# Optimization experiments

Hardware: AMD Instinct MI355X
Metric: run time of the kernel (lower is better)

## Reference

```python
import jax, jax.numpy as jnp
import numpy as np

N = 100000       # num nodes
E = 1600000      # num edges (avg degree 16)
IN, HID, OUT, C = 128, 64, 64, 16


def setup_inputs() -> dict:
    key = jax.random.key(0)
    ks = jax.random.split(key, 10)
    x = jax.random.normal(ks[0], (N, IN), jnp.float32)
    edge_index = jax.random.randint(ks[1], (2, E), 0, N, dtype=jnp.int32)
    dict_node = jax.random.randint(ks[2], (N,), 0, N, dtype=jnp.int32)
    # learned parameters (Glorot-ish scaling)
    W1 = jax.random.normal(ks[3], (IN, HID), jnp.float32) / np.sqrt(IN)
    b1 = jnp.zeros((HID,), jnp.float32)
    W2 = jax.random.normal(ks[4], (HID, OUT), jnp.float32) / np.sqrt(HID)
    b2 = jnp.zeros((OUT,), jnp.float32)
    Wfc = jax.random.normal(ks[5], (OUT, C), jnp.float32) / np.sqrt(OUT)
    bfc = jnp.zeros((C,), jnp.float32)
    return {"x": x, "edge_index": edge_index, "dict_node": dict_node,
            "W1": W1, "b1": b1, "W2": W2, "b2": b2, "Wfc": Wfc, "bfc": bfc}


def _gcn_conv(h_in, W, b, src, dst, n):
    """GCNConv: D^-1/2 (A+I) D^-1/2 (X W) + b, self-loops handled analytically."""
    h = h_in @ W                                   # [N, F]
    deg = jax.ops.segment_sum(jnp.ones((src.shape[0],), h.dtype), dst,
                              num_segments=n) + 1.0  # +1 self-loop
    dinv = jax.lax.rsqrt(deg)                      # [N]
    norm = dinv[src] * dinv[dst]                   # [E]
    agg = jax.ops.segment_sum(h[src] * norm[:, None], dst, num_segments=n)
    agg = agg + h * (dinv * dinv)[:, None]         # self-loop contribution
    return agg + b


def reference(x, edge_index, dict_node, W1, b1, W2, b2, Wfc, bfc):
    n = x.shape[0]
    src, dst = edge_index[0], edge_index[1]
    h = jax.nn.relu(_gcn_conv(x, W1, b1, src, dst, n))
    # dropout p=0.5 is identity at inference
    h = jax.nn.relu(_gcn_conv(h, W2, b2, src, dst, n))
    # global_mean_pool over dict_node with size = num_nodes
    cnt = jax.ops.segment_sum(jnp.ones((n,), h.dtype), dict_node, num_segments=n)
    summ = jax.ops.segment_sum(h, dict_node, num_segments=n)
    pooled = summ / jnp.maximum(cnt, 1.0)[:, None]
    logits = pooled @ Wfc + bfc
    return jax.nn.log_softmax(logits, axis=1)
```

## Files before the change

### kernel.cpp

```cpp
#include <hip/hip_runtime.h>

#define THREADS 256
#define KC 32
#define B1 256

typedef __attribute__((ext_vector_type(8))) short bf16x8;
typedef __attribute__((ext_vector_type(4))) float f32x4;
typedef __attribute__((ext_vector_type(2))) unsigned int u32x2;

__device__ inline ushort f2bf(float v) {
    union { float f; unsigned u; } a; a.f = v;
    unsigned r = a.u + 0x7fff + ((a.u >> 16) & 1);
    return (ushort)(r >> 16);
}
__device__ inline unsigned pack2(float a, float b) {
    return (unsigned)f2bf(a) | ((unsigned)f2bf(b) << 16);
}
__device__ inline float bflo(unsigned v) {
    union { unsigned u; float f; } a; a.u = v << 16; return a.f;
}
__device__ inline float bfhi(unsigned v) {
    union { unsigned u; float f; } a; a.u = v & 0xffff0000u; return a.f;
}


__global__ void k_p1(const int* __restrict__ dst, int* __restrict__ pc,
                     int E, int NB, int chunk) {
    __shared__ int hist[512];
    int tid = threadIdx.x, blk = blockIdx.x;
    for (int i = tid; i < NB; i += THREADS) hist[i] = 0;
    __syncthreads();
    int e0 = blk * chunk;
    int e1 = e0 + chunk; if (e1 > E) e1 = E;
    for (int e = e0 + tid; e < e1; e += THREADS)
        atomicAdd(&hist[dst[e] >> 8], 1);
    __syncthreads();
    for (int i = tid; i < NB; i += THREADS) pc[i * B1 + blk] = hist[i];
}

__global__ void k_s1(int* __restrict__ pc, int* __restrict__ bsums, int total) {
    __shared__ int s[1024];
    int t = threadIdx.x;
    int idx = blockIdx.x * 1024 + t;
    int v = (idx < total) ? pc[idx] : 0;
    s[t] = v;
    __syncthreads();
    for (int o = 1; o < 1024; o <<= 1) {
        int x = (t >= (unsigned)o) ? s[t - o] : 0;
        __syncthreads();
        s[t] += x;
        __syncthreads();
    }
    if (idx < total) pc[idx] = s[t] - v;
    if (t == 1023) bsums[blockIdx.x] = s[1023];
}

__global__ void k_s2(int* __restrict__ bsums, int nb) {
    __shared__ int s[128];
    int t = threadIdx.x;
    int v = (t < nb) ? bsums[t] : 0;
    s[t] = v;
    __syncthreads();
    for (int o = 1; o < 128; o <<= 1) {
        int x = (t >= (unsigned)o) ? s[t - o] : 0;
        __syncthreads();
        s[t] += x;
        __syncthreads();
    }
    if (t < nb) bsums[t] = s[t] - v;
}

__global__ void k_p2(const int* __restrict__ src, const int* __restrict__ dst,
                     const int* __restrict__ pc, const int* __restrict__ bsx,
                     unsigned long long* __restrict__ part, int E, int NB, int chunk) {
    __shared__ int cur[512];
    int tid = threadIdx.x, blk = blockIdx.x;
    for (int i = tid; i < NB; i += THREADS) {
        int idx = i * B1 + blk;
        cur[i] = pc[idx] + bsx[idx >> 10];
    }
    __syncthreads();
    int e0 = blk * chunk;
    int e1 = e0 + chunk; if (e1 > E) e1 = E;
    for (int e = e0 + tid; e < e1; e += THREADS) {
        int d = dst[e], sv = src[e];
        int pos = atomicAdd(&cur[d >> 8], 1);
        part[pos] = ((unsigned long long)(unsigned)d << 32) | (unsigned)sv;
    }
}

__global__ void k_p3(const unsigned long long* __restrict__ part,
                     const int* __restrict__ pc, const int* __restrict__ bsx,
                     int* __restrict__ off, float* __restrict__ dinv,
                     int* __restrict__ csr, int E, int NB, int n) {
    __shared__ int hist[256];
    __shared__ int so[256];
    int b = blockIdx.x, t = threadIdx.x;
    int i0 = b * B1, i1 = (b + 1) * B1;
    int base = pc[i0] + bsx[i0 >> 10];
    int end  = (b + 1 < NB) ? (pc[i1] + bsx[i1 >> 10]) : E;
    hist[t] = 0;
    __syncthreads();
    for (int e = base + t; e < end; e += THREADS)
        atomicAdd(&hist[(int)(part[e] >> 32) & 255], 1);
    __syncthreads();
    int h = hist[t];
    so[t] = h;
    __syncthreads();
    for (int o = 1; o < 256; o <<= 1) {
        int x = (t >= (unsigned)o) ? so[t - o] : 0;
        __syncthreads();
        so[t] += x;
        __syncthreads();
    }
    int ex = so[t] - h;
    int node = (b << 8) + t;
    if (node < n) {
        off[node]  = base + ex;
        dinv[node] = rsqrtf((float)h + 1.0f);
        if (node == n - 1) off[n] = E;
    }
    __syncthreads();
    so[t] = base + ex;
    __syncthreads();
    for (int e = base + t; e < end; e += THREADS) {
        unsigned long long p = part[e];
        int pos = atomicAdd(&so[(int)(p >> 32) & 255], 1);
        csr[pos] = (int)(p & 0xffffffffu);
    }
}

__global__ __launch_bounds__(THREADS) void
k_g1(const float* __restrict__ X, const float* __restrict__ W,
     const float* __restrict__ dinv, ushort* __restrict__ C, int n, int fin,
     const int* __restrict__ dict, float* __restrict__ cnt, int nGemm, int nCnt) {
    int tid = threadIdx.x;
    if ((int)blockIdx.x >= nGemm) {
        int stride = nCnt * THREADS;
        for (int i = ((int)blockIdx.x - nGemm) * THREADS + tid; i < n; i += stride)
            atomicAdd(&cnt[dict[i]], 1.0f);
        return;
    }
    __shared__ float Xs[KC][68];
    __shared__ float Ws[KC][64];
    int r0  = blockIdx.x * 64;
    int tx4 = (tid & 15) * 4;
    int ty4 = (tid >> 4) * 4;
    int sxr = tid >> 2, sxk = (tid & 3) * 4;
    int swk = tid >> 4, swc = (tid & 15) * 4;
    int xrow = r0 + sxr; if (xrow >= n) xrow = n - 1;
    const float* xptr = X + (size_t)xrow * fin;
    float4 acc0 = {0,0,0,0}, acc1 = {0,0,0,0}, acc2 = {0,0,0,0}, acc3 = {0,0,0,0};
    for (int kc = 0; kc < fin; kc += KC) {
        float4 xa = *(const float4*)(xptr + kc + sxk);
        float4 xb = *(const float4*)(xptr + kc + 16 + sxk);
        float4 wa = *(const float4*)(W + (size_t)(kc + swk) * 64 + swc);
        float4 wb = *(const float4*)(W + (size_t)(kc + swk + 16) * 64 + swc);
        __syncthreads();
        Xs[sxk + 0][sxr] = xa.x; Xs[sxk + 1][sxr] = xa.y;
        Xs[sxk + 2][sxr] = xa.z; Xs[sxk + 3][sxr] = xa.w;
        Xs[16 + sxk + 0][sxr] = xb.x; Xs[16 + sxk + 1][sxr] = xb.y;
        Xs[16 + sxk + 2][sxr] = xb.z; Xs[16 + sxk + 3][sxr] = xb.w;
        *(float4*)&Ws[swk][swc]      = wa;
        *(float4*)&Ws[swk + 16][swc] = wb;
        __syncthreads();
        #pragma unroll 8
        for (int k = 0; k < KC; ++k) {
            float4 a = *(const float4*)&Xs[k][ty4];
            float4 b = *(const float4*)&Ws[k][tx4];
            acc0.x = fmaf(a.x, b.x, acc0.x); acc0.y = fmaf(a.x, b.y, acc0.y);
            acc0.z = fmaf(a.x, b.z, acc0.z); acc0.w = fmaf(a.x, b.w, acc0.w);
            acc1.x = fmaf(a.y, b.x, acc1.x); acc1.y = fmaf(a.y, b.y, acc1.y);
            acc1.z = fmaf(a.y, b.z, acc1.z); acc1.w = fmaf(a.y, b.w, acc1.w);
            acc2.x = fmaf(a.z, b.x, acc2.x); acc2.y = fmaf(a.z, b.y, acc2.y);
            acc2.z = fmaf(a.z, b.z, acc2.z); acc2.w = fmaf(a.z, b.w, acc2.w);
            acc3.x = fmaf(a.w, b.x, acc3.x); acc3.y = fmaf(a.w, b.y, acc3.y);
            acc3.z = fmaf(a.w, b.z, acc3.z); acc3.w = fmaf(a.w, b.w, acc3.w);
        }
    }
    int row = r0 + ty4;
    #pragma unroll
    for (int r = 0; r < 4; ++r) {
        if (row + r >= n) break;
        float dn = dinv[row + r];
        float4 a = r == 0 ? acc0 : r == 1 ? acc1 : r == 2 ? acc2 : acc3;
        ushort4 o;
        o.x = f2bf(a.x * dn); o.y = f2bf(a.y * dn);
        o.z = f2bf(a.z * dn); o.w = f2bf(a.w * dn);
        *(ushort4*)(C + (size_t)(row + r) * 64 + tx4) = o;
    }
}

__global__ __launch_bounds__(THREADS) void
k_gemm_bf16(const ushort* __restrict__ X, const float* __restrict__ W,
            const float* __restrict__ dinv, ushort* __restrict__ C, int n, int fin) {
    __shared__ float Xs[KC][68];
    __shared__ float Ws[KC][64];
    int tid = threadIdx.x;
    int r0  = blockIdx.x * 64;
    int tx4 = (tid & 15) * 4;
    int ty4 = (tid >> 4) * 4;
    int sxr = tid >> 2, sk8 = (tid & 3) * 8;
    int swk = tid >> 4, swc = (tid & 15) * 4;
    int xrow = r0 + sxr; if (xrow >= n) xrow = n - 1;
    const ushort* xptr = X + (size_t)xrow * fin;
    float4 acc0 = {0,0,0,0}, acc1 = {0,0,0,0}, acc2 = {0,0,0,0}, acc3 = {0,0,0,0};
    for (int kc = 0; kc < fin; kc += KC) {
        uint4 xv = *(const uint4*)(xptr + kc + sk8);
        float4 wa = *(const float4*)(W + (size_t)(kc + swk) * 64 + swc);
        float4 wb = *(const float4*)(W + (size_t)(kc + swk + 16) * 64 + swc);
        __syncthreads();
        Xs[sk8 + 0][sxr] = bflo(xv.x); Xs[sk8 + 1][sxr] = bfhi(xv.x);
        Xs[sk8 + 2][sxr] = bflo(xv.y); Xs[sk8 + 3][sxr] = bfhi(xv.y);
        Xs[sk8 + 4][sxr] = bflo(xv.z); Xs[sk8 + 5][sxr] = bfhi(xv.z);
        Xs[sk8 + 6][sxr] = bflo(xv.w); Xs[sk8 + 7][sxr] = bfhi(xv.w);
        *(float4*)&Ws[swk][swc]      = wa;
        *(float4*)&Ws[swk + 16][swc] = wb;
        __syncthreads();
        #pragma unroll 8
        for (int k = 0; k < KC; ++k) {
            float4 a = *(const float4*)&Xs[k][ty4];
            float4 b = *(const float4*)&Ws[k][tx4];
            acc0.x = fmaf(a.x, b.x, acc0.x); acc0.y = fmaf(a.x, b.y, acc0.y);
            acc0.z = fmaf(a.x, b.z, acc0.z); acc0.w = fmaf(a.x, b.w, acc0.w);
            acc1.x = fmaf(a.y, b.x, acc1.x); acc1.y = fmaf(a.y, b.y, acc1.y);
            acc1.z = fmaf(a.y, b.z, acc1.z); acc1.w = fmaf(a.y, b.w, acc1.w);
            acc2.x = fmaf(a.z, b.x, acc2.x); acc2.y = fmaf(a.z, b.y, acc2.y);
            acc2.z = fmaf(a.z, b.z, acc2.z); acc2.w = fmaf(a.z, b.w, acc2.w);
            acc3.x = fmaf(a.w, b.x, acc3.x); acc3.y = fmaf(a.w, b.y, acc3.y);
            acc3.z = fmaf(a.w, b.z, acc3.z); acc3.w = fmaf(a.w, b.w, acc3.w);
        }
    }
    int row = r0 + ty4;
    #pragma unroll
    for (int r = 0; r < 4; ++r) {
        if (row + r >= n) break;
        float dn = dinv[row + r];
        float4 a = r == 0 ? acc0 : r == 1 ? acc1 : r == 2 ? acc2 : acc3;
        ushort4 o;
        o.x = f2bf(a.x * dn); o.y = f2bf(a.y * dn);
        o.z = f2bf(a.z * dn); o.w = f2bf(a.w * dn);
        *(ushort4*)(C + (size_t)(row + r) * 64 + tx4) = o;
    }
}

__device__ inline void tr_mfma4(unsigned la, const bf16x8& a,
                                f32x4& o0, f32x4& o1, f32x4& o2, f32x4& o3) {
    u32x2 r0, r1, r2, r3, r4, r5, r6, r7;
    asm volatile(
        "s_waitcnt lgkmcnt(0)\n\t"
        "ds_read_b64_tr_b16 %0, %8 offset:0\n\t"
        "ds_read_b64_tr_b16 %1, %8 offset:512\n\t"
        "ds_read_b64_tr_b16 %2, %8 offset:1024\n\t"
        "ds_read_b64_tr_b16 %3, %8 offset:1536\n\t"
        "ds_read_b64_tr_b16 %4, %8 offset:2048\n\t"
        "ds_read_b64_tr_b16 %5, %8 offset:2560\n\t"
        "ds_read_b64_tr_b16 %6, %8 offset:3072\n\t"
        "ds_read_b64_tr_b16 %7, %8 offset:3584\n\t"
        "s_waitcnt lgkmcnt(0)"
        : "=&v"(r0), "=&v"(r1), "=&v"(r2), "=&v"(r3),
          "=&v"(r4), "=&v"(r5), "=&v"(r6), "=&v"(r7)
        : "v"(la) : "memory");
    __builtin_amdgcn_sched_barrier(0);
    union { u32x2 d[2]; bf16x8 v; } b0, b1, b2, b3;
    b0.d[0] = r0; b0.d[1] = r1; b1.d[0] = r2; b1.d[1] = r3;
    b2.d[0] = r4; b2.d[1] = r5; b3.d[0] = r6; b3.d[1] = r7;
    o0 = __builtin_amdgcn_mfma_f32_16x16x32_bf16(a, b0.v, o0, 0, 0, 0);
    o1 = __builtin_amdgcn_mfma_f32_16x16x32_bf16(a, b1.v, o1, 0, 0, 0);
    o2 = __builtin_amdgcn_mfma_f32_16x16x32_bf16(a, b2.v, o2, 0, 0, 0);
    o3 = __builtin_amdgcn_mfma_f32_16x16x32_bf16(a, b3.v, o3, 0, 0, 0);
}

template<int LAYER>
__global__ __launch_bounds__(THREADS) void
k_agg(const ushort* __restrict__ H, const int* __restrict__ csr,
      const int* __restrict__ off, const float* __restrict__ dinv,
      const float* __restrict__ bias, ushort* __restrict__ outB,
      const float* __restrict__ Wfc, const int* __restrict__ dict,
      float* __restrict__ pool16, int n) {
    __shared__ ushort cbuf[4][2048];
    __shared__ float wt[16 * 65];
    int tid = threadIdx.x;
    if (LAYER == 2) {
        for (int i = tid; i < 64 * 16; i += THREADS) {
            int cc = i >> 4, r = i & 15;
            wt[r * 65 + cc] = Wfc[i];
        }
        __syncthreads();
    }
    int wslot = tid >> 6, lane = tid & 63;
    int gw = blockIdx.x * 4 + wslot;
    int n0 = gw << 4;
    if (n0 >= n) return;
    int G = lane >> 4, c16 = lane & 15;
    int g8 = lane >> 3, q = lane & 7;
    ushort* wbuf = &cbuf[wslot][0];
    unsigned lbase = (unsigned)(size_t)wbuf;
    int vm = n - n0; if (vm > 16) vm = 16;
    int sA = 0, eA = 0;
    if (c16 < vm) { sA = off[n0 + c16]; eA = off[n0 + c16 + 1]; }
    int base0   = __shfl(sA, 0);
    int baseEnd = __shfl(eA, vm - 1);
    unsigned rng = (unsigned)(eA - sA);
    int sb0 = (q >> 1) * 512 + (g8 >> 2) * 256 + (g8 & 3) * 16 + (q & 1) * 8;
    unsigned la = lbase + (unsigned)lane * 8;
    f32x4 acc0 = {0, 0, 0, 0}, acc1 = acc0, acc2 = acc0, acc3 = acc0;

    uint4 cur[4], nxt[4];
    #pragma unroll
    for (int it = 0; it < 4; ++it) {
        uint4 v = {0, 0, 0, 0};
        int k = it * 8 + g8;
        if (base0 + k < baseEnd) {
            int e = csr[base0 + k];
            v = *(const uint4*)(H + ((size_t)e << 6) + q * 8);
        }
        cur[it] = v;
    }
    for (int base = base0; base < baseEnd; base += 32) {
        #pragma unroll
        for (int it = 0; it < 4; ++it) {
            uint4 v = {0, 0, 0, 0};
            int k = base + 32 + it * 8 + g8;
            if (k < baseEnd) {
                int e = csr[k];
                v = *(const uint4*)(H + ((size_t)e << 6) + q * 8);
            }
            nxt[it] = v;
        }
        #pragma unroll
        for (int it = 0; it < 4; ++it)
            *(uint4*)(wbuf + sb0 + it * 64) = cur[it];
        int kb = base - sA;
        bf16x8 a;
        #pragma unroll
        for (int e2 = 0; e2 < 8; ++e2)
            a[e2] = ((unsigned)(G * 8 + e2 + kb) < rng) ? (short)0x3F80 : (short)0;
        tr_mfma4(la, a, acc0, acc1, acc2, acc3);
        #pragma unroll
        for (int it = 0; it < 4; ++it) cur[it] = nxt[it];
    }
    {
        #pragma unroll
        for (int it = 0; it < 4; ++it) {
            uint4 v = {0, 0, 0, 0};
            int k = it * 8 + g8;
            if (it < 2 && k < vm)
                v = *(const uint4*)(H + ((size_t)(n0 + k) << 6) + q * 8);
            *(uint4*)(wbuf + sb0 + it * 64) = v;
        }
        bf16x8 a;
        #pragma unroll
        for (int e2 = 0; e2 < 8; ++e2)
            a[e2] = ((G * 8 + e2) == c16) ? (short)0x3F80 : (short)0;
        tr_mfma4(la, a, acc0, acc1, acc2, acc3);
    }
    float* hrow = (float*)wbuf;
    float bv0 = bias[c16], bv1 = bias[c16 + 16],
          bv2 = bias[c16 + 32], bv3 = bias[c16 + 48];
    #pragma unroll
    for (int r = 0; r < 4; ++r) {
        int rr = G * 4 + r;
        if (rr < vm) {
            float dn = dinv[n0 + rr];
            float v0 = fmaxf(acc0[r] * dn + bv0, 0.f);
            float v1 = fmaxf(acc1[r] * dn + bv1, 0.f);
            float v2 = fmaxf(acc2[r] * dn + bv2, 0.f);
            float v3 = fmaxf(acc3[r] * dn + bv3, 0.f);
            hrow[rr * 64 + c16]      = v0;
            hrow[rr * 64 + c16 + 16] = v1;
            hrow[rr * 64 + c16 + 32] = v2;
            hrow[rr * 64 + c16 + 48] = v3;
        }
    }
    asm volatile("" ::: "memory");
    if (LAYER == 1) {
        int prow = lane >> 2, pseg = lane & 3;
        if (prow < vm) {
            const float* hp = hrow + prow * 64 + pseg * 16;
            float4 f0 = *(const float4*)(hp + 0);
            float4 f1 = *(const float4*)(hp + 4);
            float4 f2 = *(const float4*)(hp + 8);
            float4 f3 = *(const float4*)(hp + 12);
            uint4 o0, o1;
            o0.x = pack2(f0.x, f0.y); o0.y = pack2(f0.z, f0.w);
            o0.z = pack2(f1.x, f1.y); o0.w = pack2(f1.z, f1.w);
            o1.x = pack2(f2.x, f2.y); o1.y = pack2(f2.z, f2.w);
            o1.z = pack2(f3.x, f3.y); o1.w = pack2(f3.z, f3.w);
            ushort* op = outB + ((size_t)(n0 + prow) << 6) + pseg * 16;
            *(uint4*)(op)     = o0;
            *(uint4*)(op + 8) = o1;
        }
    } else {
        int r16 = c16;
        for (int m = 0; m < vm; ++m) {
            const float* hm = hrow + m * 64 + G * 16;
            const float* wr = wt + r16 * 65 + G * 16;
            float p = 0.f;
            #pragma unroll
            for (int i = 0; i < 16; ++i) p = fmaf(hm[i], wr[i], p);
            p += __shfl_xor(p, 16);
            p += __shfl_xor(p, 32);
            if (G == 0)
                atomicAdd(&pool16[(size_t)dict[n0 + m] * 16 + r16], p);
        }
    }
}

__global__ void k_final16(const float* __restrict__ pool16, const float* __restrict__ cnt,
                          const float* __restrict__ bfc, float* __restrict__ out, int n) {
    int tid = threadIdx.x;
    int nl = tid >> 4, lane = tid & 15;
    int node = blockIdx.x * 16 + nl;
    if (node >= n) return;
    float inv = 1.0f / fmaxf(cnt[node], 1.0f);
    float acc = pool16[(size_t)node * 16 + lane] * inv + bfc[lane];
    float m = acc;
    for (int o = 8; o; o >>= 1) m = fmaxf(m, __shfl_xor(m, o, 16));
    float ex = __expf(acc - m);
    float s = ex;
    for (int o = 8; o; o >>= 1) s += __shfl_xor(s, o, 16);
    out[(size_t)node * 16 + lane] = acc - m - __logf(s);
}

extern "C" void kernel_launch(void* const* d_in, const int* in_sizes, int n_in,
                              void* d_out, int out_size, void* d_ws, size_t ws_size,
                              hipStream_t stream) {
    const float* x    = (const float*)d_in[0];
    const int*   ei   = (const int*)d_in[1];
    const int*   dict = (const int*)d_in[2];
    const float* W1   = (const float*)d_in[3];
    const float* b1   = (const float*)d_in[4];
    const float* W2   = (const float*)d_in[5];
    const float* b2   = (const float*)d_in[6];
    const float* Wfc  = (const float*)d_in[7];
    const float* bfc  = (const float*)d_in[8];

    const int N  = in_sizes[2];
    const int E  = in_sizes[1] / 2;
    const int IN = in_sizes[0] / N;
    const int* src = ei;
    const int* dst = ei + E;

    ushort* bufA = (ushort*)d_ws;
    ushort* bufB = bufA + (size_t)N * 64;
    unsigned long long* part = (unsigned long long*)bufB;
    float* dinv    = (float*)(bufB + (size_t)N * 64);
    float* cnt     = dinv + N;
    int*   off     = (int*)(cnt + N);
    int*   pcounts = off + (N + 1);
    const int NB     = (N + 255) >> 8;
    const int pcsize = NB * B1;
    int*   bsums   = pcounts + pcsize;
    int*   csr     = bsums + 128;
    float* pool16  = (float*)(csr + E);

    const int gTile = (N + 63) / 64;
    const int gRows = (N + 15) / 16;
    const int nCnt  = 256;
    const int chunk = (E + B1 - 1) / B1;
    const int nS1   = (pcsize + 1023) >> 10;
    const int gAgg  = ((N + 15) / 16 + 3) / 4;

    hipMemsetAsync(cnt, 0, (size_t)N * sizeof(float), stream);
    hipMemsetAsync(pool16, 0, (size_t)N * 16 * sizeof(float), stream);

    k_p1<<<B1, THREADS, 0, stream>>>(dst, pcounts, E, NB, chunk);
    k_s1<<<nS1, 1024, 0, stream>>>(pcounts, bsums, pcsize);
    k_s2<<<1, 128, 0, stream>>>(bsums, nS1);
    k_p2<<<B1, THREADS, 0, stream>>>(src, dst, pcounts, bsums, part, E, NB, chunk);
    k_p3<<<NB, THREADS, 0, stream>>>(part, pcounts, bsums, off, dinv, csr, E, NB, N);

    k_g1<<<gTile + nCnt, THREADS, 0, stream>>>(x, W1, dinv, bufA, N, IN,
                                               dict, cnt, gTile, nCnt);

    k_agg<1><<<gAgg, THREADS, 0, stream>>>(bufA, csr, off, dinv, b1, bufB,
                                           nullptr, nullptr, nullptr, N);

    k_gemm_bf16<<<gTile, THREADS, 0, stream>>>(bufB, W2, dinv, bufA, N, 64);
    k_agg<2><<<gAgg, THREADS, 0, stream>>>(bufA, csr, off, dinv, b2, nullptr,
                                           Wfc, dict, pool16, N);

    k_final16<<<gRows, THREADS, 0, stream>>>(pool16, cnt, bfc, (float*)d_out, N);
}
```

Baseline: 306.0 us.

## Replace scalar FMA GEMMs with bf16 MFMA kernel using LDS weight fragments

Both dense feature transforms (X@W1 and H@W2) now go through one templated kernel. It uses 16x16x32 bf16 MFMA instructions instead of scalar fp32 FMAs tiled through shared memory. The weights are converted to bf16 and pre-swizzled into MFMA fragment layout in LDS, and each block still stages the full W. Outputs pass through a per-wave LDS tile so that rows are written as coalesced 16-byte bf16 stores. The first layer now rounds x to bf16 before multiplying, which lowers precision compared with the fp32 FMA path.

```diff
diff --git a/kernel.cpp b/kernel.cpp
--- a/kernel.cpp
+++ b/kernel.cpp
@@ -1,7 +1,6 @@
 #include <hip/hip_runtime.h>
 
 #define THREADS 256
-#define KC 32
 #define B1 256
 
 typedef __attribute__((ext_vector_type(8))) short bf16x8;
@@ -15,12 +14,6 @@
 }
 __device__ inline unsigned pack2(float a, float b) {
     return (unsigned)f2bf(a) | ((unsigned)f2bf(b) << 16);
-}
-__device__ inline float bflo(unsigned v) {
-    union { unsigned u; float f; } a; a.u = v << 16; return a.f;
-}
-__device__ inline float bfhi(unsigned v) {
-    union { unsigned u; float f; } a; a.u = v & 0xffff0000u; return a.f;
 }
 
 
@@ -130,10 +123,13 @@
     }
 }
 
+template<int KTILES, bool XF32>
 __global__ __launch_bounds__(THREADS) void
-k_g1(const float* __restrict__ X, const float* __restrict__ W,
-     const float* __restrict__ dinv, ushort* __restrict__ C, int n, int fin,
-     const int* __restrict__ dict, float* __restrict__ cnt, int nGemm, int nCnt) {
+k_mgemm(const float* __restrict__ Xf, const ushort* __restrict__ Xh,
+        const float* __restrict__ W, const float* __restrict__ dinv,
+        ushort* __restrict__ C, int n,
+        const int* __restrict__ dict, float* __restrict__ cnt,
+        int nGemm, int nCnt) {
     int tid = threadIdx.x;
     if ((int)blockIdx.x >= nGemm) {
         int stride = nCnt * THREADS;
@@ -141,106 +137,74 @@
             atomicAdd(&cnt[dict[i]], 1.0f);
         return;
     }
-    __shared__ float Xs[KC][68];
-    __shared__ float Ws[KC][64];
-    int r0  = blockIdx.x * 64;
-    int tx4 = (tid & 15) * 4;
-    int ty4 = (tid >> 4) * 4;
-    int sxr = tid >> 2, sxk = (tid & 3) * 4;
-    int swk = tid >> 4, swc = (tid & 15) * 4;
-    int xrow = r0 + sxr; if (xrow >= n) xrow = n - 1;
-    const float* xptr = X + (size_t)xrow * fin;
-    float4 acc0 = {0,0,0,0}, acc1 = {0,0,0,0}, acc2 = {0,0,0,0}, acc3 = {0,0,0,0};
-    for (int kc = 0; kc < fin; kc += KC) {
-        float4 xa = *(const float4*)(xptr + kc + sxk);
-        float4 xb = *(const float4*)(xptr + kc + 16 + sxk);
-        float4 wa = *(const float4*)(W + (size_t)(kc + swk) * 64 + swc);
-        float4 wb = *(const float4*)(W + (size_t)(kc + swk + 16) * 64 + swc);
-        __syncthreads();
-        Xs[sxk + 0][sxr] = xa.x; Xs[sxk + 1][sxr] = xa.y;
-        Xs[sxk + 2][sxr] = xa.z; Xs[sxk + 3][sxr] = xa.w;
-        Xs[16 + sxk + 0][sxr] = xb.x; Xs[16 + sxk + 1][sxr] = xb.y;
-        Xs[16 + sxk + 2][sxr] = xb.z; Xs[16 + sxk + 3][sxr] = xb.w;
-        *(float4*)&Ws[swk][swc]      = wa;
-        *(float4*)&Ws[swk + 16][swc] = wb;
-        __syncthreads();
-        #pragma unroll 8
-        for (int k = 0; k < KC; ++k) {
-            float4 a = *(const float4*)&Xs[k][ty4];
-            float4 b = *(const float4*)&Ws[k][tx4];
-            acc0.x = fmaf(a.x, b.x, acc0.x); acc0.y = fmaf(a.x, b.y, acc0.y);
-            acc0.z = fmaf(a.x, b.z, acc0.z); acc0.w = fmaf(a.x, b.w, acc0.w);
-            acc1.x = fmaf(a.y, b.x, acc1.x); acc1.y = fmaf(a.y, b.y, acc1.y);
-            acc1.z = fmaf(a.y, b.z, acc1.z); acc1.w = fmaf(a.y, b.w, acc1.w);
-            acc2.x = fmaf(a.z, b.x, acc2.x); acc2.y = fmaf(a.z, b.y, acc2.y);
-            acc2.z = fmaf(a.z, b.z, acc2.z); acc2.w = fmaf(a.z, b.w, acc2.w);
-            acc3.x = fmaf(a.w, b.x, acc3.x); acc3.y = fmaf(a.w, b.y, acc3.y);
-            acc3.z = fmaf(a.w, b.z, acc3.z); acc3.w = fmaf(a.w, b.w, acc3.w);
-        }
-    }
-    int row = r0 + ty4;
+    __shared__ ushort wfrag[KTILES * 2048];
+    __shared__ float hrow[4][16 * 64];
+    const int FIN = KTILES * 32;
+    for (int i = tid; i < FIN * 64; i += THREADS) {
+        int k = i >> 6, c = i & 63;
+        int kk = k >> 5, G = (k >> 3) & 3, e = k & 7;
+        int t = c >> 4, c16 = c & 15;
+        wfrag[(((kk * 4 + t) * 64) + G * 16 + c16) * 8 + e] = f2bf(W[i]);
+    }
+    __syncthreads();
+    int wslot = tid >> 6, lane = tid & 63;
+    int G = lane >> 4, c16 = lane & 15;
+    int n0 = blockIdx.x * 64 + wslot * 16;
+    int xrow = n0 + c16; if (xrow >= n) xrow = n - 1;
+    const bf16x8* wf = (const bf16x8*)wfrag;
+    f32x4 acc0 = {0, 0, 0, 0}, acc1 = acc0, acc2 = acc0, acc3 = acc0;
+    #pragma unroll
+    for (int kk = 0; kk < KTILES; ++kk) {
+        bf16x8 a;
+        if (XF32) {
+            const float* xp = Xf + (size_t)xrow * FIN + kk * 32 + G * 8;
+            float4 xa = *(const float4*)xp;
+            float4 xb = *(const float4*)(xp + 4);
+            a[0] = (short)f2bf(xa.x); a[1] = (short)f2bf(xa.y);
+            a[2] = (short)f2bf(xa.z); a[3] = (short)f2bf(xa.w);
+            a[4] = (short)f2bf(xb.x); a[5] = (short)f2bf(xb.y);
+            a[6] = (short)f2bf(xb.z); a[7] = (short)f2bf(xb.w);
+        } else {
+            a = *(const bf16x8*)(Xh + (size_t)xrow * FIN + kk * 32 + G * 8);
+        }
+        bf16x8 b0 = wf[(kk * 4 + 0) * 64 + lane];
+        bf16x8 b1 = wf[(kk * 4 + 1) * 64 + lane];
+        bf16x8 b2 = wf[(kk * 4 + 2) * 64 + lane];
+        bf16x8 b3 = wf[(kk * 4 + 3) * 64 + lane];
+        acc0 = __builtin_amdgcn_mfma_f32_16x16x32_bf16(a, b0, acc0, 0, 0, 0);
+        acc1 = __builtin_amdgcn_mfma_f32_16x16x32_bf16(a, b1, acc1, 0, 0, 0);
+        acc2 = __builtin_amdgcn_mfma_f32_16x16x32_bf16(a, b2, acc2, 0, 0, 0);
+        acc3 = __builtin_amdgcn_mfma_f32_16x16x32_bf16(a, b3, acc3, 0, 0, 0);
+    }
+    int vm = n - n0; if (vm > 16) vm = 16;
+    float* hr = &hrow[wslot][0];
     #pragma unroll
     for (int r = 0; r < 4; ++r) {
-        if (row + r >= n) break;
-        float dn = dinv[row + r];
-        float4 a = r == 0 ? acc0 : r == 1 ? acc1 : r == 2 ? acc2 : acc3;
-        ushort4 o;
-        o.x = f2bf(a.x * dn); o.y = f2bf(a.y * dn);
-        o.z = f2bf(a.z * dn); o.w = f2bf(a.w * dn);
-        *(ushort4*)(C + (size_t)(row + r) * 64 + tx4) = o;
-    }
-}
-
-__global__ __launch_bounds__(THREADS) void
-k_gemm_bf16(const ushort* __restrict__ X, const float* __restrict__ W,
-            const float* __restrict__ dinv, ushort* __restrict__ C, int n, int fin) {
-    __shared__ float Xs[KC][68];
-    __shared__ float Ws[KC][64];
-    int tid = threadIdx.x;
-    int r0  = blockIdx.x * 64;
-    int tx4 = (tid & 15) * 4;
-    int ty4 = (tid >> 4) * 4;
-    int sxr = tid >> 2, sk8 = (tid & 3) * 8;
-    int swk = tid >> 4, swc = (tid & 15) * 4;
-    int xrow = r0 + sxr; if (xrow >= n) xrow = n - 1;
-    const ushort* xptr = X + (size_t)xrow * fin;
-    float4 acc0 = {0,0,0,0}, acc1 = {0,0,0,0}, acc2 = {0,0,0,0}, acc3 = {0,0,0,0};
-    for (int kc = 0; kc < fin; kc += KC) {
-        uint4 xv = *(const uint4*)(xptr + kc + sk8);
-        float4 wa = *(const float4*)(W + (size_t)(kc + swk) * 64 + swc);
-        float4 wb = *(const float4*)(W + (size_t)(kc + swk + 16) * 64 + swc);
-        __syncthreads();
-        Xs[sk8 + 0][sxr] = bflo(xv.x); Xs[sk8 + 1][sxr] = bfhi(xv.x);
-        Xs[sk8 + 2][sxr] = bflo(xv.y); Xs[sk8 + 3][sxr] = bfhi(xv.y);
-        Xs[sk8 + 4][sxr] = bflo(xv.z); Xs[sk8 + 5][sxr] = bfhi(xv.z);
-        Xs[sk8 + 6][sxr] = bflo(xv.w); Xs[sk8 + 7][sxr] = bfhi(xv.w);
-        *(float4*)&Ws[swk][swc]      = wa;
-        *(float4*)&Ws[swk + 16][swc] = wb;
-        __syncthreads();
-        #pragma unroll 8
-        for (int k = 0; k < KC; ++k) {
-            float4 a = *(const float4*)&Xs[k][ty4];
-            float4 b = *(const float4*)&Ws[k][tx4];
-            acc0.x = fmaf(a.x, b.x, acc0.x); acc0.y = fmaf(a.x, b.y, acc0.y);
-            acc0.z = fmaf(a.x, b.z, acc0.z); acc0.w = fmaf(a.x, b.w, acc0.w);
-            acc1.x = fmaf(a.y, b.x, acc1.x); acc1.y = fmaf(a.y, b.y, acc1.y);
-            acc1.z = fmaf(a.y, b.z, acc1.z); acc1.w = fmaf(a.y, b.w, acc1.w);
-            acc2.x = fmaf(a.z, b.x, acc2.x); acc2.y = fmaf(a.z, b.y, acc2.y);
-            acc2.z = fmaf(a.z, b.z, acc2.z); acc2.w = fmaf(a.z, b.w, acc2.w);
-            acc3.x = fmaf(a.w, b.x, acc3.x); acc3.y = fmaf(a.w, b.y, acc3.y);
-            acc3.z = fmaf(a.w, b.z, acc3.z); acc3.w = fmaf(a.w, b.w, acc3.w);
-        }
-    }
-    int row = r0 + ty4;
-    #pragma unroll
-    for (int r = 0; r < 4; ++r) {
-        if (row + r >= n) break;
-        float dn = dinv[row + r];
-        float4 a = r == 0 ? acc0 : r == 1 ? acc1 : r == 2 ? acc2 : acc3;
-        ushort4 o;
-        o.x = f2bf(a.x * dn); o.y = f2bf(a.y * dn);
-        o.z = f2bf(a.z * dn); o.w = f2bf(a.w * dn);
-        *(ushort4*)(C + (size_t)(row + r) * 64 + tx4) = o;
+        int rr = G * 4 + r;
+        if (rr < vm) {
+            float dn = dinv[n0 + rr];
+            hr[rr * 64 + c16]      = acc0[r] * dn;
+            hr[rr * 64 + c16 + 16] = acc1[r] * dn;
+            hr[rr * 64 + c16 + 32] = acc2[r] * dn;
+            hr[rr * 64 + c16 + 48] = acc3[r] * dn;
+        }
+    }
+    asm volatile("" ::: "memory");
+    int prow = lane >> 2, pseg = lane & 3;
+    if (prow < vm) {
+        const float* hp = hr + prow * 64 + pseg * 16;
+        float4 f0 = *(const float4*)(hp + 0);
+        float4 f1 = *(const float4*)(hp + 4);
+        float4 f2 = *(const float4*)(hp + 8);
+        float4 f3 = *(const float4*)(hp + 12);
+        uint4 o0, o1;
+        o0.x = pack2(f0.x, f0.y); o0.y = pack2(f0.z, f0.w);
+        o0.z = pack2(f1.x, f1.y); o0.w = pack2(f1.z, f1.w);
+        o1.x = pack2(f2.x, f2.y); o1.y = pack2(f2.z, f2.w);
+        o1.z = pack2(f3.x, f3.y); o1.w = pack2(f3.z, f3.w);
+        ushort* op = C + ((size_t)(n0 + prow) << 6) + pseg * 16;
+        *(uint4*)(op)     = o0;
+        *(uint4*)(op + 8) = o1;
     }
 }
 
@@ -471,13 +435,14 @@
     k_p2<<<B1, THREADS, 0, stream>>>(src, dst, pcounts, bsums, part, E, NB, chunk);
     k_p3<<<NB, THREADS, 0, stream>>>(part, pcounts, bsums, off, dinv, csr, E, NB, N);
 
-    k_g1<<<gTile + nCnt, THREADS, 0, stream>>>(x, W1, dinv, bufA, N, IN,
-                                               dict, cnt, gTile, nCnt);
+    k_mgemm<4, true><<<gTile + nCnt, THREADS, 0, stream>>>(
+        x, nullptr, W1, dinv, bufA, N, dict, cnt, gTile, nCnt);
 
     k_agg<1><<<gAgg, THREADS, 0, stream>>>(bufA, csr, off, dinv, b1, bufB,
                                            nullptr, nullptr, nullptr, N);
 
-    k_gemm_bf16<<<gTile, THREADS, 0, stream>>>(bufB, W2, dinv, bufA, N, 64);
+    k_mgemm<2, false><<<gTile, THREADS, 0, stream>>>(
+        nullptr, bufB, W2, dinv, bufA, N, nullptr, nullptr, gTile, 0);
     k_agg<2><<<gAgg, THREADS, 0, stream>>>(bufA, csr, off, dinv, b2, nullptr,
                                            Wfc, dict, pool16, N);
 
```

After: 298.8 us. 2.4% less time.
